# Kernel tuning notes

Measured on AMD Instinct MI355X. Metric: run time of the kernel, lower is better.

The kernel has to match this reference:

```python
import jax, jax.numpy as jnp
import numpy as np

B, N = 8, 4096  # batch, n_nodes == hidden_size


def setup_inputs() -> dict:
    key = jax.random.key(0)
    ks = jax.random.split(key, 7)
    s = 1.0 / np.sqrt(N)  # linear-layer init scale
    return {
        "x": jax.random.normal(ks[0], (B, N), dtype=jnp.float32),
        "h": jax.random.normal(ks[1], (B, N), dtype=jnp.float32),
        "adj": jax.random.uniform(ks[2], (N, N), dtype=jnp.float32) / N,
        "W_hr": jax.random.normal(ks[3], (N, N), dtype=jnp.float32) * s,
        "b_hr": jnp.zeros((N,), dtype=jnp.float32),
        "W_hz": jax.random.normal(ks[4], (N, N), dtype=jnp.float32) * s,
        "b_hz": jnp.zeros((N,), dtype=jnp.float32),
        "W_hn": jax.random.normal(ks[5], (N, N), dtype=jnp.float32) * s,
        "b_hn": jnp.zeros((N,), dtype=jnp.float32),
    }


def reference(x, h, adj, W_hr, b_hr, W_hz, b_hz, W_hn, b_hn):
    # _gc_aggregate: matmul(adj, x[..., None]).squeeze() -> agg[b,i] = sum_j adj[i,j] x[b,j]
    agg = jnp.einsum('ij,bj->bi', adj, x)            # [B, N]
    r = jax.nn.sigmoid(agg + h @ W_hr.T + b_hr)       # reset gate
    z = jax.nn.sigmoid(agg + h @ W_hz.T + b_hz)       # update gate
    n = jnp.tanh(agg + r * (h @ W_hn.T + b_hn))       # candidate
    return (1.0 - z) * n + z * h
```

## Files before the change

kernel.cpp:

```cpp
#include <hip/hip_runtime.h>
#include <math.h>

#define NN 4096
#define BB 8
#define NV4 (NN / 4)
#define CF4 64
#define NCHUNK (NV4 / CF4)
#define ROWS 8
#define RPW 4

__global__ __launch_bounds__(512, 2) void attgru_fused_kernel(
    const float* __restrict__ x,   const float* __restrict__ h,
    const float* __restrict__ adj, const float* __restrict__ Whr,
    const float* __restrict__ bhr, const float* __restrict__ Whz,
    const float* __restrict__ bhz, const float* __restrict__ Whn,
    const float* __restrict__ bhn, float* __restrict__ out)
{
    const int t    = threadIdx.x;
    const int lane = t & 63;
    const int wave = t >> 6;
    const int gate = wave >> 1;
    const int rg   = wave & 1;
    const int row0 = blockIdx.x * ROWS;

    __shared__ float4 vbuf[2][2][BB][CF4];
    __shared__ float  red[8][RPW * BB];

    const float* Msel = (gate == 0) ? adj : (gate == 1) ? Whr
                      : (gate == 2) ? Whz : Whn;
    const int vsel = (gate != 0);
    const float4* M4 = reinterpret_cast<const float4*>(Msel)
                     + (size_t)(row0 + rg * RPW) * NV4;
    const float4* x4 = reinterpret_cast<const float4*>(x);
    const float4* h4 = reinterpret_cast<const float4*>(h);

    const int sb = t >> 6, sl = t & 63;
    const float4* srcx = x4 + sb * NV4 + sl;
    const float4* srch = h4 + sb * NV4 + sl;

    float4 mc[RPW];
#pragma unroll
    for (int r = 0; r < RPW; ++r) mc[r] = M4[r * NV4 + lane];
    {
        const float4 rx = srcx[0];
        const float4 rh = srch[0];
        vbuf[0][0][sb][sl] = rx;
        vbuf[0][1][sb][sl] = rh;
    }
    __syncthreads();

    float acc[RPW][BB];
#pragma unroll
    for (int r = 0; r < RPW; ++r)
#pragma unroll
        for (int b = 0; b < BB; ++b) acc[r][b] = 0.f;

    for (int c = 0; c < NCHUNK; ++c) {
        const int cur = c & 1, nxt = cur ^ 1;
        float4 rxn, rhn, mn[RPW];
        const bool more = (c + 1 < NCHUNK);
        if (more) {
            rxn = srcx[(c + 1) * CF4];
            rhn = srch[(c + 1) * CF4];
#pragma unroll
            for (int r = 0; r < RPW; ++r)
                mn[r] = M4[r * NV4 + (c + 1) * CF4 + lane];
        }
#pragma unroll
        for (int b = 0; b < BB; ++b) {
            const float4 vb = vbuf[cur][vsel][b][lane];
#pragma unroll
            for (int r = 0; r < RPW; ++r)
                acc[r][b] += mc[r].x * vb.x + mc[r].y * vb.y
                           + mc[r].z * vb.z + mc[r].w * vb.w;
        }
        if (more) {
            vbuf[nxt][0][sb][sl] = rxn;
            vbuf[nxt][1][sb][sl] = rhn;
#pragma unroll
            for (int r = 0; r < RPW; ++r) mc[r] = mn[r];
        }
        __syncthreads();
    }

#pragma unroll
    for (int off = 32; off >= 1; off >>= 1)
#pragma unroll
        for (int r = 0; r < RPW; ++r)
#pragma unroll
            for (int b = 0; b < BB; ++b)
                acc[r][b] += __shfl_xor(acc[r][b], off);

    if (lane == 0) {
#pragma unroll
        for (int r = 0; r < RPW; ++r)
#pragma unroll
            for (int b = 0; b < BB; ++b)
                red[wave][r * BB + b] = acc[r][b];
    }
    __syncthreads();

    if (t < ROWS * BB) {
        const int r = t >> 3, b = t & 7;
        const int rgg = r >> 2, idx = (r & 3) * BB + b;
        const int row = row0 + r;
        const float agg = red[0 * 2 + rgg][idx];
        const float rs  = red[1 * 2 + rgg][idx];
        const float zs  = red[2 * 2 + rgg][idx];
        const float ns  = red[3 * 2 + rgg][idx];
        const float rgt = 1.f / (1.f + __expf(-(agg + rs + bhr[row])));
        const float zgt = 1.f / (1.f + __expf(-(agg + zs + bhz[row])));
        const float ngt = tanhf(agg + rgt * (ns + bhn[row]));
        const float hv  = h[b * NN + row];
        out[b * NN + row] = (1.f - zgt) * ngt + zgt * hv;
    }
}

extern "C" void kernel_launch(void* const* d_in, const int* in_sizes, int n_in,
                              void* d_out, int out_size, void* d_ws, size_t ws_size,
                              hipStream_t stream) {
    const float* x   = (const float*)d_in[0];
    const float* h   = (const float*)d_in[1];
    const float* adj = (const float*)d_in[2];
    const float* Whr = (const float*)d_in[3];
    const float* bhr = (const float*)d_in[4];
    const float* Whz = (const float*)d_in[5];
    const float* bhz = (const float*)d_in[6];
    const float* Whn = (const float*)d_in[7];
    const float* bhn = (const float*)d_in[8];
    float* out = (float*)d_out;

    const int grid = NN / ROWS;
    attgru_fused_kernel<<<grid, 512, 0, stream>>>(x, h, adj, Whr, bhr, Whz, bhz,
                                                  Whn, bhn, out);
}
```

Before: 57.88 us.

## Double rows per block and split each wave into two row-groups

Each block now handles 16 rows instead of 8, and each wave splits into two 32-lane halves that each cover 4 rows, so a wave spans 8 rows. The x/h vectors are staged in larger 128-float4 chunks, so each staged vector chunk is reused across twice as many matrix rows and the grid halves. Each half-wave reduces over only 32 lanes, and matrix loads are prefetched one 32-float4 subchunk ahead. The price is fewer blocks (256) on a large GPU and smaller per-lane contiguous loads, which may reduce occupancy and memory-level parallelism.

```diff
diff --git a/kernel.cpp b/kernel.cpp
--- a/kernel.cpp
+++ b/kernel.cpp
@@ -4,10 +4,10 @@
 #define NN 4096
 #define BB 8
 #define NV4 (NN / 4)
-#define CF4 64
-#define NCHUNK (NV4 / CF4)
-#define ROWS 8
-#define RPW 4
+#define CKF4 128
+#define NCHUNK 8
+#define ROWS 16
+#define RPW 8
 
 __global__ __launch_bounds__(512, 2) void attgru_fused_kernel(
     const float* __restrict__ x,   const float* __restrict__ h,
@@ -20,99 +20,112 @@
     const int lane = t & 63;
     const int wave = t >> 6;
     const int gate = wave >> 1;
-    const int rg   = wave & 1;
+    const int half = wave & 1;
     const int row0 = blockIdx.x * ROWS;
 
-    __shared__ float4 vbuf[2][2][BB][CF4];
-    __shared__ float  red[8][RPW * BB];
+    __shared__ float4 vbuf[2][2][BB][CKF4];
+    __shared__ float  red[4][ROWS][BB];
 
     const float* Msel = (gate == 0) ? adj : (gate == 1) ? Whr
                       : (gate == 2) ? Whz : Whn;
     const int vsel = (gate != 0);
+    const int rsub = (lane >> 5) * 4;
+    const int kl   = lane & 31;
     const float4* M4 = reinterpret_cast<const float4*>(Msel)
-                     + (size_t)(row0 + rg * RPW) * NV4;
+                     + (size_t)(row0 + half * RPW + rsub) * NV4;
+
     const float4* x4 = reinterpret_cast<const float4*>(x);
     const float4* h4 = reinterpret_cast<const float4*>(h);
+    const int sb = t >> 6, sl = t & 63;
+    const float4* srcx = x4 + sb * NV4;
+    const float4* srch = h4 + sb * NV4;
 
-    const int sb = t >> 6, sl = t & 63;
-    const float4* srcx = x4 + sb * NV4 + sl;
-    const float4* srch = h4 + sb * NV4 + sl;
-
-    float4 mc[RPW];
-#pragma unroll
-    for (int r = 0; r < RPW; ++r) mc[r] = M4[r * NV4 + lane];
-    {
-        const float4 rx = srcx[0];
-        const float4 rh = srch[0];
-        vbuf[0][0][sb][sl] = rx;
-        vbuf[0][1][sb][sl] = rh;
-    }
+    vbuf[0][0][sb][sl]      = srcx[sl];
+    vbuf[0][0][sb][sl + 64] = srcx[sl + 64];
+    vbuf[0][1][sb][sl]      = srch[sl];
+    vbuf[0][1][sb][sl + 64] = srch[sl + 64];
+    float4 mc0 = M4[0 * NV4 + kl];
+    float4 mc1 = M4[1 * NV4 + kl];
+    float4 mc2 = M4[2 * NV4 + kl];
+    float4 mc3 = M4[3 * NV4 + kl];
     __syncthreads();
 
-    float acc[RPW][BB];
+    float acc[4][BB];
 #pragma unroll
-    for (int r = 0; r < RPW; ++r)
+    for (int r = 0; r < 4; ++r)
 #pragma unroll
         for (int b = 0; b < BB; ++b) acc[r][b] = 0.f;
 
     for (int c = 0; c < NCHUNK; ++c) {
-        const int cur = c & 1, nxt = cur ^ 1;
-        float4 rxn, rhn, mn[RPW];
+        const int cur = c & 1;
         const bool more = (c + 1 < NCHUNK);
+        float4 rx0, rx1, rh0, rh1;
         if (more) {
-            rxn = srcx[(c + 1) * CF4];
-            rhn = srch[(c + 1) * CF4];
-#pragma unroll
-            for (int r = 0; r < RPW; ++r)
-                mn[r] = M4[r * NV4 + (c + 1) * CF4 + lane];
+            const int vb = (c + 1) * CKF4;
+            rx0 = srcx[vb + sl];  rx1 = srcx[vb + sl + 64];
+            rh0 = srch[vb + sl];  rh1 = srch[vb + sl + 64];
         }
 #pragma unroll
-        for (int b = 0; b < BB; ++b) {
-            const float4 vb = vbuf[cur][vsel][b][lane];
+        for (int p = 0; p < 4; ++p) {
+            const int q = c * 4 + p;
+            float4 mn0, mn1, mn2, mn3;
+            if (q + 1 < 32) {
+                const int nc = (q + 1) * 32 + kl;
+                mn0 = M4[0 * NV4 + nc];  mn1 = M4[1 * NV4 + nc];
+                mn2 = M4[2 * NV4 + nc];  mn3 = M4[3 * NV4 + nc];
+            }
+            const int vk = p * 32 + kl;
 #pragma unroll
-            for (int r = 0; r < RPW; ++r)
-                acc[r][b] += mc[r].x * vb.x + mc[r].y * vb.y
-                           + mc[r].z * vb.z + mc[r].w * vb.w;
+            for (int b = 0; b < BB; ++b) {
+                const float4 v = vbuf[cur][vsel][b][vk];
+                acc[0][b] += mc0.x*v.x + mc0.y*v.y + mc0.z*v.z + mc0.w*v.w;
+                acc[1][b] += mc1.x*v.x + mc1.y*v.y + mc1.z*v.z + mc1.w*v.w;
+                acc[2][b] += mc2.x*v.x + mc2.y*v.y + mc2.z*v.z + mc2.w*v.w;
+                acc[3][b] += mc3.x*v.x + mc3.y*v.y + mc3.z*v.z + mc3.w*v.w;
+            }
+            if (q + 1 < 32) { mc0 = mn0; mc1 = mn1; mc2 = mn2; mc3 = mn3; }
         }
         if (more) {
-            vbuf[nxt][0][sb][sl] = rxn;
-            vbuf[nxt][1][sb][sl] = rhn;
-#pragma unroll
-            for (int r = 0; r < RPW; ++r) mc[r] = mn[r];
+            vbuf[cur ^ 1][0][sb][sl]      = rx0;
+            vbuf[cur ^ 1][0][sb][sl + 64] = rx1;
+            vbuf[cur ^ 1][1][sb][sl]      = rh0;
+            vbuf[cur ^ 1][1][sb][sl + 64] = rh1;
         }
         __syncthreads();
     }
 
 #pragma unroll
-    for (int off = 32; off >= 1; off >>= 1)
+    for (int off = 1; off <= 16; off <<= 1)
 #pragma unroll
-        for (int r = 0; r < RPW; ++r)
+        for (int r = 0; r < 4; ++r)
 #pragma unroll
             for (int b = 0; b < BB; ++b)
                 acc[r][b] += __shfl_xor(acc[r][b], off);
 
     if (lane == 0) {
 #pragma unroll
-        for (int r = 0; r < RPW; ++r)
+        for (int r = 0; r < 4; ++r)
 #pragma unroll
             for (int b = 0; b < BB; ++b)
-                red[wave][r * BB + b] = acc[r][b];
+                red[gate][half * RPW + r][b] = acc[r][b];
+    } else if (lane == 32) {
+#pragma unroll
+        for (int r = 0; r < 4; ++r)
+#pragma unroll
+            for (int b = 0; b < BB; ++b)
+                red[gate][half * RPW + 4 + r][b] = acc[r][b];
     }
     __syncthreads();
 
     if (t < ROWS * BB) {
         const int r = t >> 3, b = t & 7;
-        const int rgg = r >> 2, idx = (r & 3) * BB + b;
         const int row = row0 + r;
-        const float agg = red[0 * 2 + rgg][idx];
-        const float rs  = red[1 * 2 + rgg][idx];
-        const float zs  = red[2 * 2 + rgg][idx];
-        const float ns  = red[3 * 2 + rgg][idx];
-        const float rgt = 1.f / (1.f + __expf(-(agg + rs + bhr[row])));
-        const float zgt = 1.f / (1.f + __expf(-(agg + zs + bhz[row])));
-        const float ngt = tanhf(agg + rgt * (ns + bhn[row]));
-        const float hv  = h[b * NN + row];
-        out[b * NN + row] = (1.f - zgt) * ngt + zgt * hv;
+        const float agg = red[0][r][b];
+        const float rg = 1.f / (1.f + __expf(-(agg + red[1][r][b] + bhr[row])));
+        const float zg = 1.f / (1.f + __expf(-(agg + red[2][r][b] + bhz[row])));
+        const float ng = tanhf(agg + rg * (red[3][r][b] + bhn[row]));
+        const float hv = h[b * NN + row];
+        out[b * NN + row] = (1.f - zg) * ng + zg * hv;
     }
 }
 
```

Result: slower. 60.63 us (+4.8%).
